# Optimization experiments

Measured on AMD Instinct MI355X. Metric: run time of the kernel, lower is better.

Reference implementation:

```python
import jax, jax.numpy as jnp
import numpy as np

B = 64        # num_groups
G = 32        # group_size
D = 2000      # output dim (counts per bin/gene)
M = 16        # m_samples
E = 16        # noise_dim
DIN = 256
LAM = 1.0
TRUST = 0.25
SMOOTH = 1e-8
IPF_ITERS = 60
EPS = 1e-12


def _arch(x, noise, W, b):
    # simple linear architecture: concat(x, noise) @ W + b
    return jnp.concatenate([x, noise], axis=-1) @ W + b


def _loss(x, target, W, b, noise_loss):
    # replicate each row m times (unsqueeze(1).expand(...).reshape == repeat)
    x_rep = jnp.repeat(x, M, axis=0)                      # [n*M, DIN]
    pred = _arch(x_rep, noise_loss, W, b)                 # [n*M, D] (no act_fn in loss path)
    pred = pred.reshape(B, G, M, D).sum(axis=1)           # [B, M, D]
    term_conf = jnp.linalg.norm(pred - target[:, None, :], axis=2).mean(axis=1)  # [B]
    sq = jnp.sum(pred * pred, axis=2)                     # [B, M]
    inn = jnp.einsum('bmd,bnd->bmn', pred, pred)          # [B, M, M]
    sqd = jnp.clip(sq[:, :, None] + sq[:, None, :] - 2.0 * inn, 1e-6)
    d = jnp.sqrt(sqd)
    mask = 1.0 - jnp.eye(M, dtype=d.dtype)
    mean_pd = jnp.sum(d * mask, axis=(1, 2)) / (M * (M - 1))
    return jnp.mean(term_conf - (LAM / 2.0) * mean_pd)


def _ipf(x_pred, C):
    # KL/I-projection with row anchoring (keep_rows=True, trust_clip=0.25)
    y = jnp.clip(x_pred, 0.0)
    C = jnp.clip(C.astype(y.dtype), 0.0)
    R = y.sum(axis=2)                                     # [B, G] anchor row totals
    col_zero = (y.sum(axis=1) <= 0) & (C > 0)
    y = y + SMOOTH * col_zero[:, None, :].astype(y.dtype)
    row_zero = (y.sum(axis=2) <= 0) & (R > 0)
    y = y + SMOOTH * row_zero[:, :, None].astype(y.dtype)

    def body(_, y):
        col = jnp.clip(y.sum(axis=1), EPS)
        y = y * jnp.clip(C / col, 1.0 - TRUST, 1.0 + TRUST)[:, None, :]
        row = jnp.clip(y.sum(axis=2), EPS)
        y = y * jnp.clip(R / row, 1.0 - TRUST, 1.0 + TRUST)[:, :, None]
        return y

    y = jax.lax.fori_loop(0, IPF_ITERS, body, y)
    col = jnp.clip(y.sum(axis=1), EPS)
    return y * (C / col)[:, None, :]


def _rank(v, descending):
    # rank along last axis via double argsort (0 = first picked)
    order = jnp.argsort(-v if descending else v, axis=-1)
    return jnp.argsort(order, axis=-1)


def _round_to_targets(x, target_bd):
    # exact integerization across G per (B, D); jit-safe full-G rank replaces dynamic-k topk+scatter
    x = jnp.clip(x, 0.0)
    xf = jnp.floor(x)
    y = xf.astype(jnp.int32)                              # [B, G, D]
    frac = x - xf
    need = target_bd - y.sum(axis=1)                      # [B, D]
    pos = jnp.clip(need, 0)
    q = pos // G
    y = y + q[:, None, :]
    r = pos - q * G
    rank = _rank(jnp.transpose(frac, (0, 2, 1)), descending=True)   # [B, D, G]
    add = (rank < r[:, :, None]).astype(jnp.int32)
    y = y + jnp.transpose(add, (0, 2, 1))
    # negative residuals: remove from smallest frac among y > 0
    need = target_bd - y.sum(axis=1)
    neg = jnp.clip(-need, 0)
    neg = jnp.minimum(neg, y.sum(axis=1))
    q = neg // G
    y_before = y
    y = jnp.clip(y - q[:, None, :], 0)
    removed = (y_before - y).sum(axis=1)
    r = neg - removed
    frac_m = jnp.where(y > 0, frac, jnp.inf)
    rank = _rank(jnp.transpose(frac_m, (0, 2, 1)), descending=False)
    rem = (rank < r[:, :, None]).astype(jnp.int32)
    y = jnp.clip(y - jnp.transpose(rem, (0, 2, 1)), 0)
    return y


def setup_inputs() -> dict:
    key = jax.random.key(0)
    ks = jax.random.split(key, 6)
    x = jax.random.normal(ks[0], (B * G, DIN), dtype=jnp.float32)
    target = jax.random.uniform(ks[1], (B, D), dtype=jnp.float32) * 100.0
    target_sum = jax.random.randint(ks[2], (B, D), 0, 200, dtype=jnp.int32)
    W = jax.random.normal(ks[3], (DIN + E, D), dtype=jnp.float32) * 0.02
    b = jnp.zeros((D,), dtype=jnp.float32)
    noise_loss = jax.random.normal(ks[4], (B * G * M, E), dtype=jnp.float32)
    noise_sample = jax.random.normal(ks[5], (B * G, E), dtype=jnp.float32)
    return {"x": x, "target": target, "target_sum": target_sum, "W": W, "b": b,
            "noise_loss": noise_loss, "noise_sample": noise_sample}


def reference(x, target, target_sum, W, b, noise_loss, noise_sample):
    loss = _loss(x, target, W, b, noise_loss)
    # conditional_sample pipeline (no-grad in original): softplus act (min_value==0)
    x_pred = jax.nn.softplus(_arch(x, noise_sample, W, b)).reshape(B, G, D)
    y_float = _ipf(x_pred, target_sum.astype(jnp.float32))
    y_int = _round_to_targets(y_float, target_sum.astype(jnp.int32))
    return loss, y_int.reshape(B * G, D)
```

## Files before the change

### kernel.cpp

```cpp
#include <hip/hip_runtime.h>
#include <math.h>

#define NB   64
#define NG   32
#define ND   2000
#define NM   16
#define NE   16
#define NDIN 256
#define NK   272

__device__ __forceinline__ float clampf(float v, float lo, float hi) {
    return fminf(fmaxf(v, lo), hi);
}

__device__ __forceinline__ float softplusf(float v) {
    return (v > 20.f) ? v : log1pf(expf(v));
}

__device__ __forceinline__ float wave_sum32(float v[NG], int lane) {
    {   const bool hi = (lane & 32) != 0;
        #pragma unroll
        for (int k = 0; k < 16; ++k) {
            float s = hi ? v[k] : v[k + 16];
            float r = __shfl_xor(s, 32);
            v[k] = (hi ? v[k + 16] : v[k]) + r;
        }
    }
    {   const bool hi = (lane & 16) != 0;
        #pragma unroll
        for (int k = 0; k < 8; ++k) {
            float s = hi ? v[k] : v[k + 8];
            float r = __shfl_xor(s, 16);
            v[k] = (hi ? v[k + 8] : v[k]) + r;
        }
    }
    {   const bool hi = (lane & 8) != 0;
        #pragma unroll
        for (int k = 0; k < 4; ++k) {
            float s = hi ? v[k] : v[k + 4];
            float r = __shfl_xor(s, 8);
            v[k] = (hi ? v[k + 4] : v[k]) + r;
        }
    }
    {   const bool hi = (lane & 4) != 0;
        #pragma unroll
        for (int k = 0; k < 2; ++k) {
            float s = hi ? v[k] : v[k + 2];
            float r = __shfl_xor(s, 4);
            v[k] = (hi ? v[k + 2] : v[k]) + r;
        }
    }
    {   const bool hi = (lane & 2) != 0;
        float s = hi ? v[0] : v[1];
        float r = __shfl_xor(s, 2);
        v[0] = (hi ? v[1] : v[0]) + r;
    }
    v[0] += __shfl_xor(v[0], 1);
    return v[0];
}


__device__ __forceinline__ void ipf_path(
        const float* __restrict__ xp, const int* __restrict__ tsum,
        float* __restrict__ out, float* smem, int b, int t) {
    const int lane = t & 63, w = t >> 6;
    const int d0 = t * 4;
    const bool valid = (d0 < ND);
    const int g_own = (lane >> 1) & 31;

    float* wred = smem;

    float y0r[4][NG];
    #pragma unroll
    for (int g = 0; g < NG; ++g) {
        float4 v = make_float4(0.f, 0.f, 0.f, 0.f);
        if (valid) v = *(const float4*)(xp + (size_t)(b * NG + g) * ND + d0);
        y0r[0][g] = fmaxf(v.x, 0.f);
        y0r[1][g] = fmaxf(v.y, 0.f);
        y0r[2][g] = fmaxf(v.z, 0.f);
        y0r[3][g] = fmaxf(v.w, 0.f);
    }
    float Cc[4] = {0.f, 0.f, 0.f, 0.f};
    if (valid) {
        const int4 ci = *(const int4*)(tsum + (size_t)b * ND + d0);
        Cc[0] = (float)ci.x; Cc[1] = (float)ci.y; Cc[2] = (float)ci.z; Cc[3] = (float)ci.w;
    }
    float Ac[4] = {1.f, 1.f, 1.f, 1.f};
    float Bown = 1.f;
    float Rown;

    {
        float v[NG];
        #pragma unroll
        for (int g = 0; g < NG; ++g)
            v[g] = y0r[0][g] + y0r[1][g] + y0r[2][g] + y0r[3][g];
        const float tot = wave_sum32(v, lane);
        if ((lane & 1) == 0) wred[w * NG + g_own] = tot;
        __syncthreads();
        float s = 0.f;
        #pragma unroll
        for (int w2 = 0; w2 < 8; ++w2) s += wred[w2 * NG + g_own];
        Rown = s;
    }

    for (int q = 1; q <= 60; ++q) {
        float Bg[NG];
        #pragma unroll
        for (int g = 0; g < NG; ++g) Bg[g] = __shfl(Bown, 2 * g);
        float s0 = 0.f, s1 = 0.f, s2 = 0.f, s3 = 0.f;
        #pragma unroll
        for (int g = 0; g < NG; ++g) {
            const float bg = Bg[g];
            s0 += y0r[0][g] * bg; s1 += y0r[1][g] * bg;
            s2 += y0r[2][g] * bg; s3 += y0r[3][g] * bg;
        }
        Ac[0] *= clampf(Cc[0] / fmaxf(Ac[0] * s0, 1e-12f), 0.75f, 1.25f);
        Ac[1] *= clampf(Cc[1] / fmaxf(Ac[1] * s1, 1e-12f), 0.75f, 1.25f);
        Ac[2] *= clampf(Cc[2] / fmaxf(Ac[2] * s2, 1e-12f), 0.75f, 1.25f);
        Ac[3] *= clampf(Cc[3] / fmaxf(Ac[3] * s3, 1e-12f), 0.75f, 1.25f);
        float v[NG];
        #pragma unroll
        for (int g = 0; g < NG; ++g)
            v[g] = y0r[0][g] * Ac[0] + y0r[1][g] * Ac[1]
                 + y0r[2][g] * Ac[2] + y0r[3][g] * Ac[3];
        const float tot = wave_sum32(v, lane);
        const int buf = (q & 1) * (8 * NG);
        if ((lane & 1) == 0) wred[buf + w * NG + g_own] = tot;
        __syncthreads();
        float s = 0.f;
        #pragma unroll
        for (int w2 = 0; w2 < 8; ++w2) s += wred[buf + w2 * NG + g_own];
        Bown *= clampf(Rown / fmaxf(Bown * s, 1e-12f), 0.75f, 1.25f);
    }

    if (!valid) return;
    float Bg[NG];
    #pragma unroll
    for (int g = 0; g < NG; ++g) Bg[g] = __shfl(Bown, 2 * g);

    unsigned pk[NG];
    #pragma unroll
    for (int g = 0; g < NG; ++g) pk[g] = 0u;

    #pragma unroll
    for (int j = 0; j < 4; ++j) {
        float fr[NG];
        int   yv[NG];
        float s = 0.f;
        #pragma unroll
        for (int g = 0; g < NG; ++g) {
            const float z = y0r[j][g] * Ac[j] * Bg[g];
            fr[g] = z;
            s += z;
        }
        const float F = Cc[j] / fmaxf(s, 1e-12f);
        int isum = 0;
        #pragma unroll
        for (int g = 0; g < NG; ++g) {
            const float y = fr[g] * F;
            const float fl = floorf(y);
            yv[g] = (int)fl;
            fr[g] = y - fl;
            isum += yv[g];
        }
        const int Ci = (int)Cc[j];
        const int need = Ci - isum;
        const int pos = max(need, 0);
        const int q = pos >> 5;
        const int r = pos & 31;
        #pragma unroll
        for (int g = 0; g < NG; ++g) yv[g] += q;
        #pragma unroll
        for (int g = 0; g < NG; ++g) {
            int rank = 0;
            #pragma unroll
            for (int h = 0; h < NG; ++h) {
                if (h == g) continue;
                rank += (h < g) ? (fr[h] >= fr[g] ? 1 : 0) : (fr[h] > fr[g] ? 1 : 0);
            }
            if (rank < r) yv[g] += 1;
        }
        int neg = max(-need, 0);
        neg = min(neg, isum + pos);
        if (neg > 0) {
            const int q2 = neg >> 5;
            int removed = 0;
            unsigned elig = 0u;
            #pragma unroll
            for (int g = 0; g < NG; ++g) {
                const int yb = yv[g];
                const int yn = max(yb - q2, 0);
                removed += yb - yn;
                yv[g] = yn;
                if (yn > 0) elig |= (1u << g);
            }
            int r2 = neg - removed;
            for (; r2 > 0; --r2) {
                float best = __builtin_inff();
                int bi = -1;
                #pragma unroll
                for (int g = 0; g < NG; ++g) {
                    const float fm = ((elig >> g) & 1u) ? fr[g] : __builtin_inff();
                    if (fm < best) { best = fm; bi = g; }
                }
                if (bi < 0) break;
                elig &= ~(1u << bi);
                yv[bi] = max(yv[bi] - 1, 0);
            }
        }
        #pragma unroll
        for (int g = 0; g < NG; ++g)
            pk[g] |= ((unsigned)yv[g]) << (8 * j);
    }
    #pragma unroll
    for (int g = 0; g < NG; ++g) {
        float* op = &out[1 + (size_t)(b * NG + g) * ND + d0];
        op[0] = (float)(pk[g] & 0xffu);
        op[1] = (float)((pk[g] >> 8) & 0xffu);
        op[2] = (float)((pk[g] >> 16) & 0xffu);
        op[3] = (float)((pk[g] >> 24) & 0xffu);
    }
}

__device__ __forceinline__ void loss_path(
        const float* __restrict__ x, const float* __restrict__ nl,
        const float* __restrict__ tgt, const float* __restrict__ W,
        const float* __restrict__ bias, float* __restrict__ res2,
        float* smem, int cx, int b, int t) {
    float* xsl = smem;
    float* nsl = smem + 256;
    float* tgl = smem + 512;
    float* pt  = smem + 764;

    if (t < 256) {
        const float* xb = x + (size_t)b * NG * NDIN;
        float s = 0.f;
        for (int g = 0; g < NG; ++g) s += xb[g * NDIN + t];
        xsl[t] = s;
        const float* nb = nl + (size_t)b * NG * (NM * NE);
        float s2 = 0.f;
        for (int g = 0; g < NG; ++g) s2 += nb[g * (NM * NE) + t];
        nsl[t] = s2;
    }

    int tm = 0, tn = 0;
    if (t >= 16 && t < 152) {
        int p = t - 16;
        for (int m = 0; m < NM; ++m) {
            int c = NM - m;
            if (p < c) { tm = m; tn = m + p; break; }
            p -= c;
        }
    }
    __syncthreads();

    const int d = cx * 250 + t;
    if (t < 250) {
        tgl[t] = tgt[b * ND + d];
        float xw = 0.f;
        #pragma unroll 8
        for (int k = 0; k < NDIN; ++k) xw += xsl[k] * W[(size_t)k * ND + d];
        float we[NE];
        #pragma unroll
        for (int e = 0; e < NE; ++e) we[e] = W[(size_t)(NDIN + e) * ND + d];
        const float base0 = xw + (float)NG * bias[d];
        #pragma unroll
        for (int m = 0; m < NM; ++m) {
            float pm = base0;
            #pragma unroll
            for (int e = 0; e < NE; ++e) pm += nsl[m * NE + e] * we[e];
            pt[m * 252 + t] = pm;
        }
    }
    if (t < 32) {
        pt[(t >> 1) * 252 + 250 + (t & 1)] = 0.f;
        if (t < 2) tgl[250 + t] = 0.f;
    }
    __syncthreads();

    float acc = 0.f;
    if (t < 16) {
        const float4* pa  = (const float4*)&pt[t * 252];
        const float4* tga = (const float4*)&tgl[0];
        for (int i = 0; i < 63; ++i) {
            float4 pv = pa[i], tv = tga[i];
            float e0 = pv.x - tv.x, e1 = pv.y - tv.y, e2 = pv.z - tv.z, e3 = pv.w - tv.w;
            acc += e0 * e0 + e1 * e1 + e2 * e2 + e3 * e3;
        }
    } else if (t < 152) {
        const float4* pa = (const float4*)&pt[tm * 252];
        const float4* pb = (const float4*)&pt[tn * 252];
        for (int i = 0; i < 63; ++i) {
            float4 u = pa[i], v = pb[i];
            acc += u.x * v.x + u.y * v.y + u.z * v.z + u.w * v.w;
        }
    }
    if (t < 152) res2[((size_t)b * 8 + cx) * 152 + t] = acc;
}

extern "C" __global__ __launch_bounds__(512)
void mega(const float* __restrict__ x, const float* __restrict__ nl,
          const float* __restrict__ tgt, const float* __restrict__ W,
          const float* __restrict__ bias, const float* __restrict__ xp,
          const int* __restrict__ tsum, float* __restrict__ out,
          float* __restrict__ res2) {
    __shared__ float smem[4800];
    const int bid = blockIdx.x;
    const int t = threadIdx.x;
    if (bid < NB) {
        ipf_path(xp, tsum, out, smem, bid, t);
    } else {
        const int q = bid - NB;
        loss_path(x, nl, tgt, W, bias, res2, smem, q & 7, q >> 3, t);
    }
}

extern "C" __global__ __launch_bounds__(64)
void k2b_combine(const float* __restrict__ res2, float* __restrict__ out) {
    const int b = blockIdx.x, t = threadIdx.x;
    __shared__ float res[152];
    for (int tau = t; tau < 152; tau += 64) {
        float s = 0.f;
        #pragma unroll
        for (int c = 0; c < 8; ++c) s += res2[((size_t)b * 8 + c) * 152 + tau];
        res[tau] = s;
    }
    __syncthreads();
    if (t == 0) {
        float conf = 0.f;
        for (int m = 0; m < NM; ++m) conf += sqrtf(res[m]);
        conf *= (1.f / NM);
        float pd = 0.f;
        for (int m = 0; m < NM; ++m) {
            const int offm = 16 + m * NM - m * (m - 1) / 2;
            const float sqm = res[offm];
            for (int n = m + 1; n < NM; ++n) {
                const int offn = 16 + n * NM - n * (n - 1) / 2;
                const float sqn = res[offn];
                const float inn = res[offm + (n - m)];
                pd += sqrtf(fmaxf(sqm + sqn - 2.f * inn, 1e-6f));
            }
        }
        pd = 2.f * pd / (float)(NM * (NM - 1));
        atomicAdd(out, (conf - 0.5f * pd) * (1.f / NB));
    }
}

extern "C" __global__ __launch_bounds__(256)
void k3_xpred(const float* __restrict__ x, const float* __restrict__ nsamp,
              const float* __restrict__ W, const float* __restrict__ bias,
              float* __restrict__ xp) {
    const int dx = blockIdx.x;
    const int rb = blockIdx.y;
    const int t  = threadIdx.x;
    __shared__ float xr[8][NK];
    #pragma unroll
    for (int r = 0; r < 8; ++r) {
        const int row = rb * 8 + r;
        xr[r][t] = x[(size_t)row * NDIN + t];
        if (t < NE) xr[r][NDIN + t] = nsamp[row * NE + t];
    }
    __syncthreads();
    if (t >= 250) return;
    const int d = dx * 500 + 2 * t;
    float acc[8][2];
    #pragma unroll
    for (int r = 0; r < 8; ++r) { acc[r][0] = 0.f; acc[r][1] = 0.f; }
    for (int k = 0; k < NK; k += 4) {
        float2 w[4];
        #pragma unroll
        for (int kk = 0; kk < 4; ++kk) w[kk] = *(const float2*)&W[(size_t)(k + kk) * ND + d];
        #pragma unroll
        for (int r = 0; r < 8; ++r) {
            const float4 xv = *(const float4*)&xr[r][k];
            acc[r][0] += xv.x * w[0].x + xv.y * w[1].x + xv.z * w[2].x + xv.w * w[3].x;
            acc[r][1] += xv.x * w[0].y + xv.y * w[1].y + xv.z * w[2].y + xv.w * w[3].y;
        }
    }
    const float2 bv = *(const float2*)&bias[d];
    #pragma unroll
    for (int r = 0; r < 8; ++r) {
        float2 o;
        o.x = softplusf(acc[r][0] + bv.x);
        o.y = softplusf(acc[r][1] + bv.y);
        *(float2*)&xp[(size_t)(rb * 8 + r) * ND + d] = o;
    }
}

extern "C" void kernel_launch(void* const* d_in, const int* in_sizes, int n_in,
                              void* d_out, int out_size, void* d_ws, size_t ws_size,
                              hipStream_t stream) {
    const float* x     = (const float*)d_in[0];
    const float* tgt   = (const float*)d_in[1];
    const int*   tsum  = (const int*)d_in[2];
    const float* W     = (const float*)d_in[3];
    const float* bias  = (const float*)d_in[4];
    const float* nl    = (const float*)d_in[5];
    const float* nsamp = (const float*)d_in[6];
    float* out = (float*)d_out;
    float* xp  = (float*)d_ws;

    (void)in_sizes; (void)n_in; (void)out_size; (void)ws_size;

    const size_t XPB = (size_t)2048 * 2000 * 4;
    float* res2 = (float*)((char*)d_ws + XPB);

    hipMemsetAsync(d_out, 0, sizeof(float), stream);

    hipLaunchKernelGGL(k3_xpred, dim3(4, 256), dim3(256), 0, stream,
                       x, nsamp, W, bias, xp);
    hipLaunchKernelGGL(mega, dim3(NB + 512), dim3(512), 0, stream,
                       x, nl, tgt, W, bias, xp, tsum, out, res2);
    hipLaunchKernelGGL(k2b_combine, dim3(NB), dim3(64), 0, stream, res2, out);
}
```

Baseline: 318.7 us.

## Precompute group sums, widen loss chunks and xpred tiles, parallelize negative rounding

Moves the per-group x and noise sums out of every loss block into a separate k0_sums kernel, so they are computed once per group instead of once per chunk. Loss blocks now cover 500 columns each (4 chunks instead of 8). k3_xpred now computes 4 columns per thread using float4 loads of W, which halves its grid. In the IPF rounding, the serial min-search loop for removing excess units is replaced by a branchless all-pairs rank pass, and output is written directly rather than packed into bytes. Risks include an extra kernel launch, higher register pressure from the wider accumulators, and fewer loss blocks available to fill the GPU.

```diff
diff --git a/kernel.cpp b/kernel.cpp
--- a/kernel.cpp
+++ b/kernel.cpp
@@ -8,6 +8,7 @@
 #define NE   16
 #define NDIN 256
 #define NK   272
+#define NCH  4
 
 __device__ __forceinline__ float clampf(float v, float lo, float hi) {
     return fminf(fmaxf(v, lo), hi);
@@ -57,6 +58,20 @@
     }
     v[0] += __shfl_xor(v[0], 1);
     return v[0];
+}
+
+extern "C" __global__ __launch_bounds__(256)
+void k0_sums(const float* __restrict__ x, const float* __restrict__ nl,
+             float* __restrict__ sums) {
+    const int b = blockIdx.x, t = threadIdx.x;
+    const float* xb = x + (size_t)b * NG * NDIN;
+    float s = 0.f;
+    for (int g = 0; g < NG; ++g) s += xb[g * NDIN + t];
+    sums[(size_t)b * 512 + t] = s;
+    const float* nb = nl + (size_t)b * NG * (NM * NE);
+    float s2 = 0.f;
+    for (int g = 0; g < NG; ++g) s2 += nb[g * (NM * NE) + t];
+    sums[(size_t)b * 512 + 256 + t] = s2;
 }
 
 
@@ -138,10 +153,6 @@
     #pragma unroll
     for (int g = 0; g < NG; ++g) Bg[g] = __shfl(Bown, 2 * g);
 
-    unsigned pk[NG];
-    #pragma unroll
-    for (int g = 0; g < NG; ++g) pk[g] = 0u;
-
     #pragma unroll
     for (int j = 0; j < 4; ++j) {
         float fr[NG];
@@ -181,66 +192,52 @@
             if (rank < r) yv[g] += 1;
         }
         int neg = max(-need, 0);
-        neg = min(neg, isum + pos);
-        if (neg > 0) {
+        neg = min(neg, isum);
+        if (__builtin_expect(neg > 0, 0)) {
             const int q2 = neg >> 5;
             int removed = 0;
-            unsigned elig = 0u;
             #pragma unroll
             for (int g = 0; g < NG; ++g) {
                 const int yb = yv[g];
                 const int yn = max(yb - q2, 0);
                 removed += yb - yn;
                 yv[g] = yn;
-                if (yn > 0) elig |= (1u << g);
             }
-            int r2 = neg - removed;
-            for (; r2 > 0; --r2) {
-                float best = __builtin_inff();
-                int bi = -1;
+            const int r2 = neg - removed;
+            if (r2 > 0) {
+                const float INF = __builtin_inff();
                 #pragma unroll
                 for (int g = 0; g < NG; ++g) {
-                    const float fm = ((elig >> g) & 1u) ? fr[g] : __builtin_inff();
-                    if (fm < best) { best = fm; bi = g; }
+                    const float fg = (yv[g] > 0) ? fr[g] : INF;
+                    int rank = 0;
+                    #pragma unroll
+                    for (int h = 0; h < NG; ++h) {
+                        if (h == g) continue;
+                        const float fh = (yv[h] > 0) ? fr[h] : INF;
+                        rank += (h < g) ? (fh <= fg ? 1 : 0) : (fh < fg ? 1 : 0);
+                    }
+                    if (rank < r2) yv[g] = max(yv[g] - 1, 0);
                 }
-                if (bi < 0) break;
-                elig &= ~(1u << bi);
-                yv[bi] = max(yv[bi] - 1, 0);
             }
         }
         #pragma unroll
         for (int g = 0; g < NG; ++g)
-            pk[g] |= ((unsigned)yv[g]) << (8 * j);
-    }
-    #pragma unroll
-    for (int g = 0; g < NG; ++g) {
-        float* op = &out[1 + (size_t)(b * NG + g) * ND + d0];
-        op[0] = (float)(pk[g] & 0xffu);
-        op[1] = (float)((pk[g] >> 8) & 0xffu);
-        op[2] = (float)((pk[g] >> 16) & 0xffu);
-        op[3] = (float)((pk[g] >> 24) & 0xffu);
+            out[1 + (size_t)(b * NG + g) * ND + (d0 + j)] = (float)yv[g];
     }
 }
 
 __device__ __forceinline__ void loss_path(
-        const float* __restrict__ x, const float* __restrict__ nl,
-        const float* __restrict__ tgt, const float* __restrict__ W,
-        const float* __restrict__ bias, float* __restrict__ res2,
-        float* smem, int cx, int b, int t) {
+        const float* __restrict__ sums, const float* __restrict__ tgt,
+        const float* __restrict__ W, const float* __restrict__ bias,
+        float* __restrict__ res2, float* smem, int cx, int b, int t) {
     float* xsl = smem;
     float* nsl = smem + 256;
     float* tgl = smem + 512;
-    float* pt  = smem + 764;
+    float* pt  = smem + 1016;
 
     if (t < 256) {
-        const float* xb = x + (size_t)b * NG * NDIN;
-        float s = 0.f;
-        for (int g = 0; g < NG; ++g) s += xb[g * NDIN + t];
-        xsl[t] = s;
-        const float* nb = nl + (size_t)b * NG * (NM * NE);
-        float s2 = 0.f;
-        for (int g = 0; g < NG; ++g) s2 += nb[g * (NM * NE) + t];
-        nsl[t] = s2;
+        xsl[t] = sums[(size_t)b * 512 + t];
+        nsl[t] = sums[(size_t)b * 512 + 256 + t];
     }
 
     int tm = 0, tn = 0;
@@ -254,8 +251,8 @@
     }
     __syncthreads();
 
-    const int d = cx * 250 + t;
-    if (t < 250) {
+    const int d = cx * 500 + t;
+    if (t < 500) {
         tgl[t] = tgt[b * ND + d];
         float xw = 0.f;
         #pragma unroll 8
@@ -269,49 +266,48 @@
             float pm = base0;
             #pragma unroll
             for (int e = 0; e < NE; ++e) pm += nsl[m * NE + e] * we[e];
-            pt[m * 252 + t] = pm;
-        }
-    }
-    if (t < 32) {
-        pt[(t >> 1) * 252 + 250 + (t & 1)] = 0.f;
-        if (t < 2) tgl[250 + t] = 0.f;
+            pt[m * 504 + t] = pm;
+        }
+    }
+    if (t < 64) {
+        pt[(t >> 2) * 504 + 500 + (t & 3)] = 0.f;
+        if (t < 4) tgl[500 + t] = 0.f;
     }
     __syncthreads();
 
     float acc = 0.f;
     if (t < 16) {
-        const float4* pa  = (const float4*)&pt[t * 252];
+        const float4* pa  = (const float4*)&pt[t * 504];
         const float4* tga = (const float4*)&tgl[0];
-        for (int i = 0; i < 63; ++i) {
+        for (int i = 0; i < 126; ++i) {
             float4 pv = pa[i], tv = tga[i];
             float e0 = pv.x - tv.x, e1 = pv.y - tv.y, e2 = pv.z - tv.z, e3 = pv.w - tv.w;
             acc += e0 * e0 + e1 * e1 + e2 * e2 + e3 * e3;
         }
     } else if (t < 152) {
-        const float4* pa = (const float4*)&pt[tm * 252];
-        const float4* pb = (const float4*)&pt[tn * 252];
-        for (int i = 0; i < 63; ++i) {
+        const float4* pa = (const float4*)&pt[tm * 504];
+        const float4* pb = (const float4*)&pt[tn * 504];
+        for (int i = 0; i < 126; ++i) {
             float4 u = pa[i], v = pb[i];
             acc += u.x * v.x + u.y * v.y + u.z * v.z + u.w * v.w;
         }
     }
-    if (t < 152) res2[((size_t)b * 8 + cx) * 152 + t] = acc;
-}
-
-extern "C" __global__ __launch_bounds__(512)
-void mega(const float* __restrict__ x, const float* __restrict__ nl,
-          const float* __restrict__ tgt, const float* __restrict__ W,
-          const float* __restrict__ bias, const float* __restrict__ xp,
-          const int* __restrict__ tsum, float* __restrict__ out,
-          float* __restrict__ res2) {
-    __shared__ float smem[4800];
+    if (t < 152) res2[((size_t)b * NCH + cx) * 152 + t] = acc;
+}
+
+extern "C" __global__ __launch_bounds__(512, 2)
+void mega(const float* __restrict__ sums, const float* __restrict__ tgt,
+          const float* __restrict__ W, const float* __restrict__ bias,
+          const float* __restrict__ xp, const int* __restrict__ tsum,
+          float* __restrict__ out, float* __restrict__ res2) {
+    __shared__ float smem[9080];
     const int bid = blockIdx.x;
     const int t = threadIdx.x;
     if (bid < NB) {
         ipf_path(xp, tsum, out, smem, bid, t);
     } else {
         const int q = bid - NB;
-        loss_path(x, nl, tgt, W, bias, res2, smem, q & 7, q >> 3, t);
+        loss_path(sums, tgt, W, bias, res2, smem, q & 3, q >> 2, t);
     }
 }
 
@@ -322,7 +318,7 @@
     for (int tau = t; tau < 152; tau += 64) {
         float s = 0.f;
         #pragma unroll
-        for (int c = 0; c < 8; ++c) s += res2[((size_t)b * 8 + c) * 152 + tau];
+        for (int c = 0; c < NCH; ++c) s += res2[((size_t)b * NCH + c) * 152 + tau];
         res[tau] = s;
     }
     __syncthreads();
@@ -362,28 +358,34 @@
     }
     __syncthreads();
     if (t >= 250) return;
-    const int d = dx * 500 + 2 * t;
-    float acc[8][2];
-    #pragma unroll
-    for (int r = 0; r < 8; ++r) { acc[r][0] = 0.f; acc[r][1] = 0.f; }
+    const int d = dx * 1000 + 4 * t;
+    float acc[8][4];
+    #pragma unroll
+    for (int r = 0; r < 8; ++r) {
+        acc[r][0] = 0.f; acc[r][1] = 0.f; acc[r][2] = 0.f; acc[r][3] = 0.f;
+    }
     for (int k = 0; k < NK; k += 4) {
-        float2 w[4];
-        #pragma unroll
-        for (int kk = 0; kk < 4; ++kk) w[kk] = *(const float2*)&W[(size_t)(k + kk) * ND + d];
+        float4 w[4];
+        #pragma unroll
+        for (int kk = 0; kk < 4; ++kk) w[kk] = *(const float4*)&W[(size_t)(k + kk) * ND + d];
         #pragma unroll
         for (int r = 0; r < 8; ++r) {
             const float4 xv = *(const float4*)&xr[r][k];
             acc[r][0] += xv.x * w[0].x + xv.y * w[1].x + xv.z * w[2].x + xv.w * w[3].x;
             acc[r][1] += xv.x * w[0].y + xv.y * w[1].y + xv.z * w[2].y + xv.w * w[3].y;
-        }
-    }
-    const float2 bv = *(const float2*)&bias[d];
+            acc[r][2] += xv.x * w[0].z + xv.y * w[1].z + xv.z * w[2].z + xv.w * w[3].z;
+            acc[r][3] += xv.x * w[0].w + xv.y * w[1].w + xv.z * w[2].w + xv.w * w[3].w;
+        }
+    }
+    const float4 bv = *(const float4*)&bias[d];
     #pragma unroll
     for (int r = 0; r < 8; ++r) {
-        float2 o;
+        float4 o;
         o.x = softplusf(acc[r][0] + bv.x);
         o.y = softplusf(acc[r][1] + bv.y);
-        *(float2*)&xp[(size_t)(rb * 8 + r) * ND + d] = o;
+        o.z = softplusf(acc[r][2] + bv.z);
+        o.w = softplusf(acc[r][3] + bv.w);
+        *(float4*)&xp[(size_t)(rb * 8 + r) * ND + d] = o;
     }
 }
 
@@ -402,14 +404,17 @@
 
     (void)in_sizes; (void)n_in; (void)out_size; (void)ws_size;
 
-    const size_t XPB = (size_t)2048 * 2000 * 4;
+    const size_t XPB  = (size_t)2048 * 2000 * 4;
+    const size_t RESB = (size_t)NB * NCH * 152 * 4;
     float* res2 = (float*)((char*)d_ws + XPB);
+    float* sums = (float*)((char*)d_ws + XPB + RESB);
 
     hipMemsetAsync(d_out, 0, sizeof(float), stream);
 
-    hipLaunchKernelGGL(k3_xpred, dim3(4, 256), dim3(256), 0, stream,
+    hipLaunchKernelGGL(k0_sums, dim3(NB), dim3(256), 0, stream, x, nl, sums);
+    hipLaunchKernelGGL(k3_xpred, dim3(2, 256), dim3(256), 0, stream,
                        x, nsamp, W, bias, xp);
-    hipLaunchKernelGGL(mega, dim3(NB + 512), dim3(512), 0, stream,
-                       x, nl, tgt, W, bias, xp, tsum, out, res2);
+    hipLaunchKernelGGL(mega, dim3(NB + NB * NCH), dim3(512), 0, stream,
+                       sums, tgt, W, bias, xp, tsum, out, res2);
     hipLaunchKernelGGL(k2b_combine, dim3(NB), dim3(64), 0, stream, res2, out);
 }
```

New measurement: 555.8 us. 1.74x slower.

## Use readlane broadcasts, rank-based decrement, wider xpred tiles, occupancy hint

Applied to the files above, without the earlier changes.

Replaces per-iteration __shfl broadcasts of the row scale with scalar readlane calls inside the IPF loop and the final rounding. The serial argmin loop for removing excess counts becomes a branch-free pairwise ranking, and the neg clamp now uses isum instead of isum+pos. The xpred GEMM kernel has each thread compute 4 columns with float4 loads and launches half as many blocks. A min-blocks hint is added to the mega kernel's launch bounds. The readlane change assumes a constant lane index, and the new rounding path changes tie and clamp behaviour slightly.

```diff
diff --git a/kernel.cpp b/kernel.cpp
--- a/kernel.cpp
+++ b/kernel.cpp
@@ -17,6 +17,10 @@
     return (v > 20.f) ? v : log1pf(expf(v));
 }
 
+__device__ __forceinline__ float readlane_f(float v, int lane) {
+    return __int_as_float(__builtin_amdgcn_readlane(__float_as_int(v), lane));
+}
+
 __device__ __forceinline__ float wave_sum32(float v[NG], int lane) {
     {   const bool hi = (lane & 32) != 0;
         #pragma unroll
@@ -104,13 +108,10 @@
     }
 
     for (int q = 1; q <= 60; ++q) {
-        float Bg[NG];
-        #pragma unroll
-        for (int g = 0; g < NG; ++g) Bg[g] = __shfl(Bown, 2 * g);
         float s0 = 0.f, s1 = 0.f, s2 = 0.f, s3 = 0.f;
         #pragma unroll
         for (int g = 0; g < NG; ++g) {
-            const float bg = Bg[g];
+            const float bg = readlane_f(Bown, 2 * g);
             s0 += y0r[0][g] * bg; s1 += y0r[1][g] * bg;
             s2 += y0r[2][g] * bg; s3 += y0r[3][g] * bg;
         }
@@ -134,9 +135,6 @@
     }
 
     if (!valid) return;
-    float Bg[NG];
-    #pragma unroll
-    for (int g = 0; g < NG; ++g) Bg[g] = __shfl(Bown, 2 * g);
 
     unsigned pk[NG];
     #pragma unroll
@@ -149,7 +147,7 @@
         float s = 0.f;
         #pragma unroll
         for (int g = 0; g < NG; ++g) {
-            const float z = y0r[j][g] * Ac[j] * Bg[g];
+            const float z = y0r[j][g] * Ac[j] * readlane_f(Bown, 2 * g);
             fr[g] = z;
             s += z;
         }
@@ -181,31 +179,32 @@
             if (rank < r) yv[g] += 1;
         }
         int neg = max(-need, 0);
-        neg = min(neg, isum + pos);
-        if (neg > 0) {
+        neg = min(neg, isum);
+        if (__builtin_expect(neg > 0, 0)) {
             const int q2 = neg >> 5;
             int removed = 0;
-            unsigned elig = 0u;
             #pragma unroll
             for (int g = 0; g < NG; ++g) {
                 const int yb = yv[g];
                 const int yn = max(yb - q2, 0);
                 removed += yb - yn;
                 yv[g] = yn;
-                if (yn > 0) elig |= (1u << g);
             }
-            int r2 = neg - removed;
-            for (; r2 > 0; --r2) {
-                float best = __builtin_inff();
-                int bi = -1;
+            const int r2 = neg - removed;
+            if (r2 > 0) {
+                const float INF = __builtin_inff();
                 #pragma unroll
                 for (int g = 0; g < NG; ++g) {
-                    const float fm = ((elig >> g) & 1u) ? fr[g] : __builtin_inff();
-                    if (fm < best) { best = fm; bi = g; }
+                    const float fg = (yv[g] > 0) ? fr[g] : INF;
+                    int rank = 0;
+                    #pragma unroll
+                    for (int h = 0; h < NG; ++h) {
+                        if (h == g) continue;
+                        const float fh = (yv[h] > 0) ? fr[h] : INF;
+                        rank += (h < g) ? (fh <= fg ? 1 : 0) : (fh < fg ? 1 : 0);
+                    }
+                    if (rank < r2) yv[g] = max(yv[g] - 1, 0);
                 }
-                if (bi < 0) break;
-                elig &= ~(1u << bi);
-                yv[bi] = max(yv[bi] - 1, 0);
             }
         }
         #pragma unroll
@@ -298,7 +297,7 @@
     if (t < 152) res2[((size_t)b * 8 + cx) * 152 + t] = acc;
 }
 
-extern "C" __global__ __launch_bounds__(512)
+extern "C" __global__ __launch_bounds__(512, 1)
 void mega(const float* __restrict__ x, const float* __restrict__ nl,
           const float* __restrict__ tgt, const float* __restrict__ W,
           const float* __restrict__ bias, const float* __restrict__ xp,
@@ -362,28 +361,34 @@
     }
     __syncthreads();
     if (t >= 250) return;
-    const int d = dx * 500 + 2 * t;
-    float acc[8][2];
-    #pragma unroll
-    for (int r = 0; r < 8; ++r) { acc[r][0] = 0.f; acc[r][1] = 0.f; }
+    const int d = dx * 1000 + 4 * t;
+    float acc[8][4];
+    #pragma unroll
+    for (int r = 0; r < 8; ++r) {
+        acc[r][0] = 0.f; acc[r][1] = 0.f; acc[r][2] = 0.f; acc[r][3] = 0.f;
+    }
     for (int k = 0; k < NK; k += 4) {
-        float2 w[4];
-        #pragma unroll
-        for (int kk = 0; kk < 4; ++kk) w[kk] = *(const float2*)&W[(size_t)(k + kk) * ND + d];
+        float4 w[4];
+        #pragma unroll
+        for (int kk = 0; kk < 4; ++kk) w[kk] = *(const float4*)&W[(size_t)(k + kk) * ND + d];
         #pragma unroll
         for (int r = 0; r < 8; ++r) {
             const float4 xv = *(const float4*)&xr[r][k];
             acc[r][0] += xv.x * w[0].x + xv.y * w[1].x + xv.z * w[2].x + xv.w * w[3].x;
             acc[r][1] += xv.x * w[0].y + xv.y * w[1].y + xv.z * w[2].y + xv.w * w[3].y;
-        }
-    }
-    const float2 bv = *(const float2*)&bias[d];
+            acc[r][2] += xv.x * w[0].z + xv.y * w[1].z + xv.z * w[2].z + xv.w * w[3].z;
+            acc[r][3] += xv.x * w[0].w + xv.y * w[1].w + xv.z * w[2].w + xv.w * w[3].w;
+        }
+    }
+    const float4 bv = *(const float4*)&bias[d];
     #pragma unroll
     for (int r = 0; r < 8; ++r) {
-        float2 o;
+        float4 o;
         o.x = softplusf(acc[r][0] + bv.x);
         o.y = softplusf(acc[r][1] + bv.y);
-        *(float2*)&xp[(size_t)(rb * 8 + r) * ND + d] = o;
+        o.z = softplusf(acc[r][2] + bv.z);
+        o.w = softplusf(acc[r][3] + bv.w);
+        *(float4*)&xp[(size_t)(rb * 8 + r) * ND + d] = o;
     }
 }
 
@@ -407,7 +412,7 @@
 
     hipMemsetAsync(d_out, 0, sizeof(float), stream);
 
-    hipLaunchKernelGGL(k3_xpred, dim3(4, 256), dim3(256), 0, stream,
+    hipLaunchKernelGGL(k3_xpred, dim3(2, 256), dim3(256), 0, stream,
                        x, nsamp, W, bias, xp);
     hipLaunchKernelGGL(mega, dim3(NB + 512), dim3(512), 0, stream,
                        x, nl, tgt, W, bias, xp, tsum, out, res2);
```

Measured after the change: 316.7 us. No clear change (-0.6%).
